# Optimization experiments

Hardware: AMD Instinct MI355X
Metric: run time of the kernel (lower is better)

## Reference

```python
import jax, jax.numpy as jnp
import numpy as np

N = 4096          # number of agents
TOP_K = 12        # config.TOP_K
OBS_RADIUS = 1.0  # config.OBS_RADIUS


def setup_inputs() -> dict:
    key = jax.random.key(0)
    ks = jax.random.split(key, 10)

    def lin(k, o, i):
        return jax.random.normal(k, (o, i), dtype=jnp.float32) * (1.0 / np.sqrt(i))

    x = jax.random.normal(ks[0], (N, N, 4), dtype=jnp.float32)
    r = jnp.asarray(0.25, dtype=jnp.float32)  # safety radius subtracted from d_norm
    W1 = lin(ks[1], 64, 6);   b1 = jax.random.normal(ks[2], (64,), jnp.float32) * 0.01
    W2 = lin(ks[3], 128, 64); b2 = jax.random.normal(ks[4], (128,), jnp.float32) * 0.01
    W3 = lin(ks[5], 64, 128); b3 = jax.random.normal(ks[6], (64,), jnp.float32) * 0.01
    W4 = lin(ks[7], 1, 64);   b4 = jax.random.normal(ks[8], (1,), jnp.float32) * 0.01
    return {"x": x, "r": r, "W1": W1, "b1": b1, "W2": W2, "b2": b2,
            "W3": W3, "b3": b3, "W4": W4, "b4": b4}


def reference(x, r, W1, b1, W2, b2, W3, b3, W4, b4):
    n = x.shape[0]
    # d_norm with eps added INSIDE the sum (matches torch: sum(x**2 + 1e-4))
    d_norm = jnp.sqrt(jnp.sum(x[:, :, :2] ** 2 + 0.0001, axis=2, keepdims=True))  # [n,n,1]
    eye = jnp.eye(n, dtype=x.dtype)[:, :, None]                                   # [n,n,1]
    xf = jnp.concatenate([x, eye, d_norm - r], axis=2)                            # [n,n,6]

    # remove_distant_agents: top-k nearest by 2D norm (eps 1e-6 inside sum)
    dn = jnp.sqrt(jnp.sum(xf[:, :, :2] ** 2 + 1e-06, axis=2))                     # [n,n]
    _, idx = jax.lax.top_k(-dn, TOP_K)                                            # [n,K]
    xg = jnp.take_along_axis(xf, idx[:, :, None], axis=1)                         # [n,K,6]

    dist = jnp.sqrt(jnp.sum(xg[:, :, :2] ** 2 + 0.0001, axis=2, keepdims=True))   # [n,K,1]
    mask = (dist <= OBS_RADIUS).astype(xg.dtype)

    # 1x1 Conv1d stack == per-neighbor MLP
    h = jax.nn.relu(jnp.einsum('nkc,oc->nko', xg, W1) + b1)
    h = jax.nn.relu(jnp.einsum('nkc,oc->nko', h, W2) + b2)
    h = jax.nn.relu(jnp.einsum('nkc,oc->nko', h, W3) + b3)
    out = (jnp.einsum('nkc,oc->nko', h, W4) + b4) * mask                          # [n,K,1]

    rows = jnp.broadcast_to(jnp.arange(n)[:, None], (n, TOP_K))
    indices = jnp.stack([rows, idx], axis=2).reshape(-1, 2)                       # [n*K,2]
    return out, mask, indices
```

## Files before the change

### kernel.cpp

```cpp
#include <hip/hip_runtime.h>

#define NN    4096
#define TOPK  12
#define NP    (NN * TOPK)
#define OFF_MASK (NP)
#define OFF_IDX  (2 * NP)

__device__ __forceinline__ unsigned long long bitonic64(unsigned long long key, int lane) {
    #pragma unroll
    for (int k = 2; k <= 64; k <<= 1) {
        #pragma unroll
        for (int jj = k >> 1; jj >= 1; jj >>= 1) {
            unsigned long long ok = __shfl_xor(key, jj, 64);
            bool keepMin = ((lane & k) == 0) == ((lane & jj) == 0);
            unsigned long long mn = (ok < key) ? ok : key;
            unsigned long long mx = (ok < key) ? key : ok;
            key = keepMin ? mn : mx;
        }
    }
    return key;
}

__global__ __launch_bounds__(256, 6) void topk_rows(const float* __restrict__ x,
                                                    float* __restrict__ out) {
    const int i    = blockIdx.x;
    const int t    = threadIdx.x;
    const int lane = t & 63;
    const int w    = t >> 6;
    const float4* x4 = (const float4*)x + (size_t)i * NN;

    float s[16];
    #pragma unroll
    for (int k = 0; k < 16; ++k) {
        float4 v = x4[(k << 8) + t];
        s[k] = v.x * v.x + v.y * v.y;
    }

    float bs = s[0]; int bj = t;
    #pragma unroll
    for (int k = 1; k < 16; ++k) {
        int j = (k << 8) + t;
        if (s[k] < bs) { bs = s[k]; bj = j; }
    }
    unsigned long long bk =
        ((unsigned long long)__float_as_uint(bs) << 32) | (unsigned)bj;

    __shared__ unsigned long long cand[64];
    __shared__ unsigned long long wtop[4 * TOPK];
    __shared__ float Tsh;
    __shared__ int   cnt[4];

    {
        unsigned long long key = bitonic64(bk, lane);
        if (lane < TOPK) wtop[w * TOPK + lane] = key;
    }
    __syncthreads();

    if (w == 0) {
        unsigned long long k2 = (lane < 4 * TOPK) ? wtop[lane] : ~0ULL;
        k2 = bitonic64(k2, lane);
        if (lane == TOPK - 1) Tsh = __uint_as_float((unsigned)(k2 >> 32));
    }
    __syncthreads();
    const float T = Tsh;

    int c = 0;
    #pragma unroll
    for (int k = 0; k < 16; ++k) c += (s[k] <= T) ? 1 : 0;

    int pfx = c;
    #pragma unroll
    for (int off = 1; off < 64; off <<= 1) {
        int o = __shfl_up(pfx, off, 64);
        if (lane >= off) pfx += o;
    }
    if (lane == 63) cnt[w] = pfx;
    __syncthreads();

    const int total = cnt[0] + cnt[1] + cnt[2] + cnt[3];

    if (total <= 64) {
        int base = 0;
        for (int ww = 0; ww < w; ++ww) base += cnt[ww];
        int o = base + (pfx - c);
        #pragma unroll
        for (int k = 0; k < 16; ++k) {
            if (s[k] <= T)
                cand[o++] = ((unsigned long long)__float_as_uint(s[k]) << 32)
                            | (unsigned)((k << 8) + t);
        }
        __syncthreads();

        if (w == 0) {
            unsigned long long k3 = (lane < total) ? cand[lane] : ~0ULL;
            k3 = bitonic64(k3, lane);
            if (lane < TOPK) {
                int   j  = (int)(k3 & 0xffffffffULL);
                float ss = __uint_as_float((unsigned)(k3 >> 32));
                float d  = sqrtf(ss + 2.0e-4f);
                float m  = (d <= 1.0f) ? 1.0f : 0.0f;
                int p = i * TOPK + lane;
                out[OFF_MASK + p]        = m;
                out[OFF_IDX + 2 * p]     = (float)i;
                out[OFF_IDX + 2 * p + 1] = (float)j;
            }
        }
        return;
    }

    unsigned long long mykey = ~0ULL;
    for (int it = 0; it < TOPK; ++it) {
        unsigned long long vk = bk;
        #pragma unroll
        for (int off = 1; off < 64; off <<= 1) {
            unsigned long long ok = __shfl_xor(vk, off, 64);
            vk = (ok < vk) ? ok : vk;
        }
        if (lane == it) mykey = vk;
        int wj = (int)(vk & 0xffffffffULL);
        if ((wj & 63) == lane) {
            int kk = wj >> 8;
            #pragma unroll
            for (int k = 0; k < 16; ++k)
                if (k == kk) s[k] = 3.0e38f;
            float nbs = s[0]; int nbj = t;
            #pragma unroll
            for (int k = 1; k < 16; ++k) {
                int j = (k << 8) + t;
                if (s[k] < nbs) { nbs = s[k]; nbj = j; }
            }
            bk = ((unsigned long long)__float_as_uint(nbs) << 32) | (unsigned)nbj;
        }
    }
    if (lane < TOPK) cand[w * TOPK + lane] = mykey;
    __syncthreads();

    if (w == 0) {
        unsigned long long k3 = (lane < 4 * TOPK) ? cand[lane] : ~0ULL;
        k3 = bitonic64(k3, lane);
        if (lane < TOPK) {
            int   j  = (int)(k3 & 0xffffffffULL);
            float ss = __uint_as_float((unsigned)(k3 >> 32));
            float d  = sqrtf(ss + 2.0e-4f);
            float m  = (d <= 1.0f) ? 1.0f : 0.0f;
            int p = i * TOPK + lane;
            out[OFF_MASK + p]        = m;
            out[OFF_IDX + 2 * p]     = (float)i;
            out[OFF_IDX + 2 * p + 1] = (float)j;
        }
    }
}

__global__ __launch_bounds__(512, 6) void mlp_block(
        const float* __restrict__ x, const float* __restrict__ rp,
        const float* __restrict__ W1, const float* __restrict__ b1,
        const float* __restrict__ W2, const float* __restrict__ b2,
        const float* __restrict__ W3, const float* __restrict__ b3,
        const float* __restrict__ W4, const float* __restrict__ b4,
        float* out) {
    __shared__ float h1s[64 * 64];
    __shared__ float h2s[128 * 64];
    __shared__ float p4s[8 * 64];

    const int t  = threadIdx.x;
    const int pl = t & 63;
    const int ch = __builtin_amdgcn_readfirstlane(t >> 6);
    const int p  = blockIdx.x * 64 + pl;
    const int i  = p / TOPK;
    const int j  = (int)out[OFF_IDX + 2 * p + 1];

    const float4 v = ((const float4*)x)[(size_t)i * NN + j];
    const float d  = sqrtf(v.x * v.x + v.y * v.y + 2.0e-4f);
    float xin[6];
    xin[0] = v.x; xin[1] = v.y; xin[2] = v.z; xin[3] = v.w;
    xin[4] = (i == j) ? 1.0f : 0.0f;
    xin[5] = d - rp[0];

    #pragma unroll
    for (int q = 0; q < 8; ++q) {
        int m = ch * 8 + q;
        const float* w = W1 + m * 6;
        float a = b1[m];
        #pragma unroll
        for (int c = 0; c < 6; ++c) a += w[c] * xin[c];
        h1s[m * 64 + pl] = fmaxf(a, 0.0f);
    }
    __syncthreads();

    float acc[16];
    #pragma unroll
    for (int q = 0; q < 16; ++q) acc[q] = b2[ch * 16 + q];
    for (int part = 0; part < 4; ++part) {
        float h1r[16];
        #pragma unroll
        for (int k = 0; k < 16; ++k) h1r[k] = h1s[(part * 16 + k) * 64 + pl];
        #pragma unroll
        for (int q = 0; q < 16; ++q) {
            const float* w = W2 + (ch * 16 + q) * 64 + part * 16;
            #pragma unroll
            for (int k = 0; k < 16; ++k) acc[q] += w[k] * h1r[k];
        }
    }
    #pragma unroll
    for (int q = 0; q < 16; ++q) h2s[(ch * 16 + q) * 64 + pl] = fmaxf(acc[q], 0.0f);
    __syncthreads();

    float h3[8];
    #pragma unroll
    for (int q = 0; q < 8; ++q) h3[q] = b3[ch * 8 + q];
    for (int part = 0; part < 8; ++part) {
        float h2r[16];
        #pragma unroll
        for (int k = 0; k < 16; ++k) h2r[k] = h2s[(part * 16 + k) * 64 + pl];
        #pragma unroll
        for (int q = 0; q < 8; ++q) {
            const float* w = W3 + (ch * 8 + q) * 128 + part * 16;
            #pragma unroll
            for (int k = 0; k < 16; ++k) h3[q] += w[k] * h2r[k];
        }
    }
    float partial = 0.0f;
    #pragma unroll
    for (int q = 0; q < 8; ++q) partial += W4[ch * 8 + q] * fmaxf(h3[q], 0.0f);
    p4s[ch * 64 + pl] = partial;
    __syncthreads();

    if (t < 64) {
        float s = b4[0];
        #pragma unroll
        for (int c = 0; c < 8; ++c) s += p4s[c * 64 + t];
        int pp = blockIdx.x * 64 + t;
        out[pp] = s * out[OFF_MASK + pp];
    }
}

extern "C" void kernel_launch(void* const* d_in, const int* in_sizes, int n_in,
                              void* d_out, int out_size, void* d_ws, size_t ws_size,
                              hipStream_t stream) {
    const float* x  = (const float*)d_in[0];
    const float* rp = (const float*)d_in[1];
    const float* W1 = (const float*)d_in[2];
    const float* b1 = (const float*)d_in[3];
    const float* W2 = (const float*)d_in[4];
    const float* b2 = (const float*)d_in[5];
    const float* W3 = (const float*)d_in[6];
    const float* b3 = (const float*)d_in[7];
    const float* W4 = (const float*)d_in[8];
    const float* b4 = (const float*)d_in[9];
    float* out = (float*)d_out;

    topk_rows<<<NN, 256, 0, stream>>>(x, out);
    mlp_block<<<NP / 64, 512, 0, stream>>>(x, rp, W1, b1, W2, b2, W3, b3, W4, b4, out);
}
```

Measured before the change: 405.2 us.

## Fuse top-k selection and per-neighbor MLP into a single kernel

Merges the top-k kernel and the MLP kernel into one launch, where each row's block runs the 12-neighbor MLP right after selection, using the top-12 keys kept in shared memory. This removes the second launch, the round trip of indices through global memory, and the gather re-read of x by a separate kernel. The cost is that only 192 of 256 threads work during the MLP, and the block keeps extra shared memory and registers, which may lower occupancy in the bandwidth-bound top-k phase.

```diff
diff --git a/kernel.cpp b/kernel.cpp
--- a/kernel.cpp
+++ b/kernel.cpp
@@ -21,8 +21,13 @@
     return key;
 }
 
-__global__ __launch_bounds__(256, 6) void topk_rows(const float* __restrict__ x,
-                                                    float* __restrict__ out) {
+__global__ __launch_bounds__(256, 6) void cbf_fused(
+        const float* __restrict__ x, const float* __restrict__ rp,
+        const float* __restrict__ W1, const float* __restrict__ b1,
+        const float* __restrict__ W2, const float* __restrict__ b2,
+        const float* __restrict__ W3, const float* __restrict__ b3,
+        const float* __restrict__ W4, const float* __restrict__ b4,
+        float* __restrict__ out) {
     const int i    = blockIdx.x;
     const int t    = threadIdx.x;
     const int lane = t & 63;
@@ -47,8 +52,12 @@
 
     __shared__ unsigned long long cand[64];
     __shared__ unsigned long long wtop[4 * TOPK];
+    __shared__ unsigned long long top12[TOPK];
     __shared__ float Tsh;
     __shared__ int   cnt[4];
+    __shared__ __align__(16) float h1sh[TOPK][68];
+    __shared__ __align__(16) float h2sh[TOPK][132];
+    __shared__ __align__(16) float p4sh[TOPK][16];
 
     {
         unsigned long long key = bitonic64(bk, lane);
@@ -95,6 +104,7 @@
             unsigned long long k3 = (lane < total) ? cand[lane] : ~0ULL;
             k3 = bitonic64(k3, lane);
             if (lane < TOPK) {
+                top12[lane] = k3;
                 int   j  = (int)(k3 & 0xffffffffULL);
                 float ss = __uint_as_float((unsigned)(k3 >> 32));
                 float d  = sqrtf(ss + 2.0e-4f);
@@ -105,132 +115,128 @@
                 out[OFF_IDX + 2 * p + 1] = (float)j;
             }
         }
-        return;
-    }
-
-    unsigned long long mykey = ~0ULL;
-    for (int it = 0; it < TOPK; ++it) {
-        unsigned long long vk = bk;
-        #pragma unroll
-        for (int off = 1; off < 64; off <<= 1) {
-            unsigned long long ok = __shfl_xor(vk, off, 64);
-            vk = (ok < vk) ? ok : vk;
-        }
-        if (lane == it) mykey = vk;
-        int wj = (int)(vk & 0xffffffffULL);
-        if ((wj & 63) == lane) {
-            int kk = wj >> 8;
-            #pragma unroll
-            for (int k = 0; k < 16; ++k)
-                if (k == kk) s[k] = 3.0e38f;
-            float nbs = s[0]; int nbj = t;
-            #pragma unroll
-            for (int k = 1; k < 16; ++k) {
-                int j = (k << 8) + t;
-                if (s[k] < nbs) { nbs = s[k]; nbj = j; }
-            }
-            bk = ((unsigned long long)__float_as_uint(nbs) << 32) | (unsigned)nbj;
-        }
-    }
-    if (lane < TOPK) cand[w * TOPK + lane] = mykey;
-    __syncthreads();
-
-    if (w == 0) {
-        unsigned long long k3 = (lane < 4 * TOPK) ? cand[lane] : ~0ULL;
-        k3 = bitonic64(k3, lane);
-        if (lane < TOPK) {
-            int   j  = (int)(k3 & 0xffffffffULL);
-            float ss = __uint_as_float((unsigned)(k3 >> 32));
-            float d  = sqrtf(ss + 2.0e-4f);
-            float m  = (d <= 1.0f) ? 1.0f : 0.0f;
-            int p = i * TOPK + lane;
-            out[OFF_MASK + p]        = m;
-            out[OFF_IDX + 2 * p]     = (float)i;
-            out[OFF_IDX + 2 * p + 1] = (float)j;
-        }
-    }
-}
-
-__global__ __launch_bounds__(512, 6) void mlp_block(
-        const float* __restrict__ x, const float* __restrict__ rp,
-        const float* __restrict__ W1, const float* __restrict__ b1,
-        const float* __restrict__ W2, const float* __restrict__ b2,
-        const float* __restrict__ W3, const float* __restrict__ b3,
-        const float* __restrict__ W4, const float* __restrict__ b4,
-        float* out) {
-    __shared__ float h1s[64 * 64];
-    __shared__ float h2s[128 * 64];
-    __shared__ float p4s[8 * 64];
-
-    const int t  = threadIdx.x;
-    const int pl = t & 63;
-    const int ch = __builtin_amdgcn_readfirstlane(t >> 6);
-    const int p  = blockIdx.x * 64 + pl;
-    const int i  = p / TOPK;
-    const int j  = (int)out[OFF_IDX + 2 * p + 1];
-
-    const float4 v = ((const float4*)x)[(size_t)i * NN + j];
-    const float d  = sqrtf(v.x * v.x + v.y * v.y + 2.0e-4f);
+    } else {
+        unsigned long long mykey = ~0ULL;
+        for (int it = 0; it < TOPK; ++it) {
+            unsigned long long vk = bk;
+            #pragma unroll
+            for (int off = 1; off < 64; off <<= 1) {
+                unsigned long long ok = __shfl_xor(vk, off, 64);
+                vk = (ok < vk) ? ok : vk;
+            }
+            if (lane == it) mykey = vk;
+            int wj = (int)(vk & 0xffffffffULL);
+            if ((wj & 63) == lane) {
+                int kk = wj >> 8;
+                #pragma unroll
+                for (int k = 0; k < 16; ++k)
+                    if (k == kk) s[k] = 3.0e38f;
+                float nbs = s[0]; int nbj = t;
+                #pragma unroll
+                for (int k = 1; k < 16; ++k) {
+                    int j = (k << 8) + t;
+                    if (s[k] < nbs) { nbs = s[k]; nbj = j; }
+                }
+                bk = ((unsigned long long)__float_as_uint(nbs) << 32) | (unsigned)nbj;
+            }
+        }
+        if (lane < TOPK) cand[w * TOPK + lane] = mykey;
+        __syncthreads();
+
+        if (w == 0) {
+            unsigned long long k3 = (lane < 4 * TOPK) ? cand[lane] : ~0ULL;
+            k3 = bitonic64(k3, lane);
+            if (lane < TOPK) {
+                top12[lane] = k3;
+                int   j  = (int)(k3 & 0xffffffffULL);
+                float ss = __uint_as_float((unsigned)(k3 >> 32));
+                float d  = sqrtf(ss + 2.0e-4f);
+                float m  = (d <= 1.0f) ? 1.0f : 0.0f;
+                int p = i * TOPK + lane;
+                out[OFF_MASK + p]        = m;
+                out[OFF_IDX + 2 * p]     = (float)i;
+                out[OFF_IDX + 2 * p + 1] = (float)j;
+            }
+        }
+    }
+    __syncthreads();
+
+    const bool act = (t < 192);
+    const int p = t >> 4;
+    const int l = t & 15;
+
     float xin[6];
-    xin[0] = v.x; xin[1] = v.y; xin[2] = v.z; xin[3] = v.w;
-    xin[4] = (i == j) ? 1.0f : 0.0f;
-    xin[5] = d - rp[0];
-
-    #pragma unroll
-    for (int q = 0; q < 8; ++q) {
-        int m = ch * 8 + q;
-        const float* w = W1 + m * 6;
-        float a = b1[m];
-        #pragma unroll
-        for (int c = 0; c < 6; ++c) a += w[c] * xin[c];
-        h1s[m * 64 + pl] = fmaxf(a, 0.0f);
-    }
-    __syncthreads();
-
-    float acc[16];
-    #pragma unroll
-    for (int q = 0; q < 16; ++q) acc[q] = b2[ch * 16 + q];
-    for (int part = 0; part < 4; ++part) {
-        float h1r[16];
-        #pragma unroll
-        for (int k = 0; k < 16; ++k) h1r[k] = h1s[(part * 16 + k) * 64 + pl];
-        #pragma unroll
-        for (int q = 0; q < 16; ++q) {
-            const float* w = W2 + (ch * 16 + q) * 64 + part * 16;
-            #pragma unroll
-            for (int k = 0; k < 16; ++k) acc[q] += w[k] * h1r[k];
-        }
-    }
-    #pragma unroll
-    for (int q = 0; q < 16; ++q) h2s[(ch * 16 + q) * 64 + pl] = fmaxf(acc[q], 0.0f);
-    __syncthreads();
-
-    float h3[8];
-    #pragma unroll
-    for (int q = 0; q < 8; ++q) h3[q] = b3[ch * 8 + q];
-    for (int part = 0; part < 8; ++part) {
-        float h2r[16];
-        #pragma unroll
-        for (int k = 0; k < 16; ++k) h2r[k] = h2s[(part * 16 + k) * 64 + pl];
-        #pragma unroll
-        for (int q = 0; q < 8; ++q) {
-            const float* w = W3 + (ch * 8 + q) * 128 + part * 16;
-            #pragma unroll
-            for (int k = 0; k < 16; ++k) h3[q] += w[k] * h2r[k];
-        }
-    }
-    float partial = 0.0f;
-    #pragma unroll
-    for (int q = 0; q < 8; ++q) partial += W4[ch * 8 + q] * fmaxf(h3[q], 0.0f);
-    p4s[ch * 64 + pl] = partial;
-    __syncthreads();
-
-    if (t < 64) {
-        float s = b4[0];
-        #pragma unroll
-        for (int c = 0; c < 8; ++c) s += p4s[c * 64 + t];
-        int pp = blockIdx.x * 64 + t;
-        out[pp] = s * out[OFF_MASK + pp];
+    float m = 0.0f;
+    if (act) {
+        const unsigned long long key = top12[p];
+        const int   j  = (int)(key & 0xffffffffULL);
+        const float ss = __uint_as_float((unsigned)(key >> 32));
+        const float d  = sqrtf(ss + 2.0e-4f);
+        m = (d <= 1.0f) ? 1.0f : 0.0f;
+
+        const float4 v = x4[j];
+        xin[0] = v.x; xin[1] = v.y; xin[2] = v.z; xin[3] = v.w;
+        xin[4] = (i == j) ? 1.0f : 0.0f;
+        xin[5] = d - rp[0];
+
+        #pragma unroll
+        for (int n = 0; n < 4; ++n) {
+            int q = l * 4 + n;
+            float a = b1[q];
+            #pragma unroll
+            for (int cc = 0; cc < 6; ++cc) a += W1[q * 6 + cc] * xin[cc];
+            h1sh[p][q] = fmaxf(a, 0.0f);
+        }
+    }
+    __syncthreads();
+
+    if (act) {
+        float acc2[8];
+        #pragma unroll
+        for (int n = 0; n < 8; ++n) acc2[n] = b2[l * 8 + n];
+        const float4* h1f4 = (const float4*)&h1sh[p][0];
+        const float4* w2f4 = (const float4*)W2;
+        #pragma unroll
+        for (int kk = 0; kk < 16; ++kk) {
+            float4 hv = h1f4[kk];
+            #pragma unroll
+            for (int n = 0; n < 8; ++n) {
+                float4 wv = w2f4[(l * 8 + n) * 16 + kk];
+                acc2[n] += wv.x * hv.x + wv.y * hv.y + wv.z * hv.z + wv.w * hv.w;
+            }
+        }
+        #pragma unroll
+        for (int n = 0; n < 8; ++n) h2sh[p][l * 8 + n] = fmaxf(acc2[n], 0.0f);
+    }
+    __syncthreads();
+
+    if (act) {
+        float acc3[4];
+        #pragma unroll
+        for (int n = 0; n < 4; ++n) acc3[n] = b3[l * 4 + n];
+        const float4* h2f4 = (const float4*)&h2sh[p][0];
+        const float4* w3f4 = (const float4*)W3;
+        #pragma unroll
+        for (int kk = 0; kk < 32; ++kk) {
+            float4 hv = h2f4[kk];
+            #pragma unroll
+            for (int n = 0; n < 4; ++n) {
+                float4 wv = w3f4[(l * 4 + n) * 32 + kk];
+                acc3[n] += wv.x * hv.x + wv.y * hv.y + wv.z * hv.z + wv.w * hv.w;
+            }
+        }
+        float partial = 0.0f;
+        #pragma unroll
+        for (int n = 0; n < 4; ++n) partial += W4[l * 4 + n] * fmaxf(acc3[n], 0.0f);
+        p4sh[p][l] = partial;
+    }
+    __syncthreads();
+
+    if (act && l == 0) {
+        float sum = b4[0];
+        #pragma unroll
+        for (int cc = 0; cc < 16; ++cc) sum += p4sh[p][cc];
+        out[i * TOPK + p] = sum * m;
     }
 }
 
@@ -249,6 +255,5 @@
     const float* b4 = (const float*)d_in[9];
     float* out = (float*)d_out;
 
-    topk_rows<<<NN, 256, 0, stream>>>(x, out);
-    mlp_block<<<NP / 64, 512, 0, stream>>>(x, rp, W1, b1, W2, b2, W3, b3, W4, b4, out);
+    cbf_fused<<<NN, 256, 0, stream>>>(x, rp, W1, b1, W2, b2, W3, b3, W4, b4, out);
 }
```

Result: slower. 713.4 us (+76.1%).

## Fuse top-k and MLP into one persistent pipelined kernel with flag handoff

Applied to the files above, without the earlier changes.

Merges the top-k row selection and the per-neighbor MLP into a single launch. Blocks are grouped so that 16 blocks compute top-k rows and 3 blocks run the MLP on those rows. The MLP blocks wait on per-element ready flags in workspace and recompute any row whose flag never arrives within a spin limit. This removes the second launch and the round trip of indices and mask through global memory, and lets the two stages overlap. In exchange it adds a memset, spin-wait polling, and halves MLP block width to 256 threads.

```diff
diff --git a/kernel.cpp b/kernel.cpp
--- a/kernel.cpp
+++ b/kernel.cpp
@@ -5,6 +5,10 @@
 #define NP    (NN * TOPK)
 #define OFF_MASK (NP)
 #define OFF_IDX  (2 * NP)
+
+#define GROUPS 256
+#define GRID   (GROUPS * 19)
+#define SPIN   10000
 
 __device__ __forceinline__ unsigned long long bitonic64(unsigned long long key, int lane) {
     #pragma unroll
@@ -21,10 +25,11 @@
     return key;
 }
 
-__global__ __launch_bounds__(256, 6) void topk_rows(const float* __restrict__ x,
-                                                    float* __restrict__ out) {
-    const int i    = blockIdx.x;
-    const int t    = threadIdx.x;
+__device__ __forceinline__ void topk_one_row(
+        const float* __restrict__ x, float* __restrict__ out,
+        int* __restrict__ wsf, int i, int t,
+        unsigned long long* cand, unsigned long long* wtop,
+        float* Tsh, int* cnt) {
     const int lane = t & 63;
     const int w    = t >> 6;
     const float4* x4 = (const float4*)x + (size_t)i * NN;
@@ -35,7 +40,6 @@
         float4 v = x4[(k << 8) + t];
         s[k] = v.x * v.x + v.y * v.y;
     }
-
     float bs = s[0]; int bj = t;
     #pragma unroll
     for (int k = 1; k < 16; ++k) {
@@ -45,11 +49,6 @@
     unsigned long long bk =
         ((unsigned long long)__float_as_uint(bs) << 32) | (unsigned)bj;
 
-    __shared__ unsigned long long cand[64];
-    __shared__ unsigned long long wtop[4 * TOPK];
-    __shared__ float Tsh;
-    __shared__ int   cnt[4];
-
     {
         unsigned long long key = bitonic64(bk, lane);
         if (lane < TOPK) wtop[w * TOPK + lane] = key;
@@ -59,15 +58,14 @@
     if (w == 0) {
         unsigned long long k2 = (lane < 4 * TOPK) ? wtop[lane] : ~0ULL;
         k2 = bitonic64(k2, lane);
-        if (lane == TOPK - 1) Tsh = __uint_as_float((unsigned)(k2 >> 32));
-    }
-    __syncthreads();
-    const float T = Tsh;
+        if (lane == TOPK - 1) *Tsh = __uint_as_float((unsigned)(k2 >> 32));
+    }
+    __syncthreads();
+    const float T = *Tsh;
 
     int c = 0;
     #pragma unroll
     for (int k = 0; k < 16; ++k) c += (s[k] <= T) ? 1 : 0;
-
     int pfx = c;
     #pragma unroll
     for (int off = 1; off < 64; off <<= 1) {
@@ -89,148 +87,193 @@
                 cand[o++] = ((unsigned long long)__float_as_uint(s[k]) << 32)
                             | (unsigned)((k << 8) + t);
         }
-        __syncthreads();
-
-        if (w == 0) {
-            unsigned long long k3 = (lane < total) ? cand[lane] : ~0ULL;
-            k3 = bitonic64(k3, lane);
-            if (lane < TOPK) {
-                int   j  = (int)(k3 & 0xffffffffULL);
-                float ss = __uint_as_float((unsigned)(k3 >> 32));
-                float d  = sqrtf(ss + 2.0e-4f);
-                float m  = (d <= 1.0f) ? 1.0f : 0.0f;
-                int p = i * TOPK + lane;
-                out[OFF_MASK + p]        = m;
-                out[OFF_IDX + 2 * p]     = (float)i;
-                out[OFF_IDX + 2 * p + 1] = (float)j;
-            }
-        }
-        return;
-    }
-
-    unsigned long long mykey = ~0ULL;
-    for (int it = 0; it < TOPK; ++it) {
-        unsigned long long vk = bk;
-        #pragma unroll
-        for (int off = 1; off < 64; off <<= 1) {
-            unsigned long long ok = __shfl_xor(vk, off, 64);
-            vk = (ok < vk) ? ok : vk;
-        }
-        if (lane == it) mykey = vk;
-        int wj = (int)(vk & 0xffffffffULL);
-        if ((wj & 63) == lane) {
-            int kk = wj >> 8;
-            #pragma unroll
-            for (int k = 0; k < 16; ++k)
-                if (k == kk) s[k] = 3.0e38f;
-            float nbs = s[0]; int nbj = t;
-            #pragma unroll
-            for (int k = 1; k < 16; ++k) {
-                int j = (k << 8) + t;
-                if (s[k] < nbs) { nbs = s[k]; nbj = j; }
-            }
-            bk = ((unsigned long long)__float_as_uint(nbs) << 32) | (unsigned)nbj;
-        }
-    }
-    if (lane < TOPK) cand[w * TOPK + lane] = mykey;
-    __syncthreads();
-
+    } else {
+        unsigned long long mykey = ~0ULL;
+        for (int it = 0; it < TOPK; ++it) {
+            unsigned long long vk = bk;
+            #pragma unroll
+            for (int off = 1; off < 64; off <<= 1) {
+                unsigned long long ok = __shfl_xor(vk, off, 64);
+                vk = (ok < vk) ? ok : vk;
+            }
+            if (lane == it) mykey = vk;
+            int wj = (int)(vk & 0xffffffffULL);
+            if ((wj & 63) == lane) {
+                int kk = wj >> 8;
+                #pragma unroll
+                for (int k = 0; k < 16; ++k)
+                    if (k == kk) s[k] = 3.0e38f;
+                float nbs = s[0]; int nbj = t;
+                #pragma unroll
+                for (int k = 1; k < 16; ++k) {
+                    int j = (k << 8) + t;
+                    if (s[k] < nbs) { nbs = s[k]; nbj = j; }
+                }
+                bk = ((unsigned long long)__float_as_uint(nbs) << 32) | (unsigned)nbj;
+            }
+        }
+        if (lane < TOPK) cand[w * TOPK + lane] = mykey;
+    }
+    __syncthreads();
+
+    const int n = (total <= 64) ? total : (4 * TOPK);
     if (w == 0) {
-        unsigned long long k3 = (lane < 4 * TOPK) ? cand[lane] : ~0ULL;
+        unsigned long long k3 = (lane < n) ? cand[lane] : ~0ULL;
         k3 = bitonic64(k3, lane);
         if (lane < TOPK) {
             int   j  = (int)(k3 & 0xffffffffULL);
             float ss = __uint_as_float((unsigned)(k3 >> 32));
             float d  = sqrtf(ss + 2.0e-4f);
-            float m  = (d <= 1.0f) ? 1.0f : 0.0f;
+            int   mb = (d <= 1.0f) ? 1 : 0;
             int p = i * TOPK + lane;
-            out[OFF_MASK + p]        = m;
+            out[OFF_MASK + p]        = (float)mb;
             out[OFF_IDX + 2 * p]     = (float)i;
             out[OFF_IDX + 2 * p + 1] = (float)j;
-        }
-    }
-}
-
-__global__ __launch_bounds__(512, 6) void mlp_block(
+            atomicExch(&wsf[i * TOPK + lane], (j << 2) | (mb << 1) | 1);
+        }
+    }
+}
+
+__global__ __launch_bounds__(256, 3) void cbf_pipe(
         const float* __restrict__ x, const float* __restrict__ rp,
         const float* __restrict__ W1, const float* __restrict__ b1,
         const float* __restrict__ W2, const float* __restrict__ b2,
         const float* __restrict__ W3, const float* __restrict__ b3,
         const float* __restrict__ W4, const float* __restrict__ b4,
-        float* out) {
-    __shared__ float h1s[64 * 64];
+        float* __restrict__ out, int* __restrict__ wsf) {
+    __shared__ __align__(16) float h1s[64 * 64];
     __shared__ float h2s[128 * 64];
     __shared__ float p4s[8 * 64];
-
-    const int t  = threadIdx.x;
+    __shared__ int   jmj[6 * TOPK];
+    __shared__ float jmm[6 * TOPK];
+    __shared__ int   nrdy[6];
+
+    unsigned long long* cand = (unsigned long long*)h1s;
+    unsigned long long* wtop = cand + 64;
+    float* Tsh = (float*)(wtop + 4 * TOPK);
+    int*   cnt = (int*)(Tsh + 1);
+
+    const int g    = blockIdx.x;
+    const int t    = threadIdx.x;
+    const int G    = g / 19;
+    const int role = g % 19;
+
+    if (role < 16) {
+        topk_one_row(x, out, wsf, G * 16 + role, t, cand, wtop, Tsh, cnt);
+        return;
+    }
+
+    const int mb = G * 3 + (role - 16);
+    const int r0 = (mb * 64) / TOPK;
+
+    if (t < 6) nrdy[t] = 0;
+    __syncthreads();
+    if (t < 72) {
+        int* f = &wsf[(r0 + t / TOPK) * TOPK + (t % TOPK)];
+        int v = 0;
+        for (int it = 0; it < SPIN; ++it) {
+            v = atomicAdd(f, 0);
+            if (v) break;
+            __builtin_amdgcn_s_sleep(4);
+        }
+        if (!v) nrdy[t / TOPK] = 1;
+    }
+    __syncthreads();
+    for (int r = 0; r < 6; ++r) {
+        if (nrdy[r]) {
+            topk_one_row(x, out, wsf, r0 + r, t, cand, wtop, Tsh, cnt);
+            __syncthreads();
+        }
+    }
+    if (t < 72) {
+        int v = atomicAdd(&wsf[(r0 + t / TOPK) * TOPK + (t % TOPK)], 0);
+        jmj[t] = v >> 2;
+        jmm[t] = ((v >> 1) & 1) ? 1.0f : 0.0f;
+    }
+    __syncthreads();
+
     const int pl = t & 63;
-    const int ch = __builtin_amdgcn_readfirstlane(t >> 6);
-    const int p  = blockIdx.x * 64 + pl;
-    const int i  = p / TOPK;
-    const int j  = (int)out[OFF_IDX + 2 * p + 1];
-
-    const float4 v = ((const float4*)x)[(size_t)i * NN + j];
+    const int wv = t >> 6;
+    const int p  = mb * 64 + pl;
+    const int ip = p / TOPK;
+    const int li = ip - r0;
+    const int kk = p % TOPK;
+    const int jj = jmj[li * TOPK + kk];
+
+    const float4 v = ((const float4*)x)[(size_t)ip * NN + jj];
     const float d  = sqrtf(v.x * v.x + v.y * v.y + 2.0e-4f);
     float xin[6];
     xin[0] = v.x; xin[1] = v.y; xin[2] = v.z; xin[3] = v.w;
-    xin[4] = (i == j) ? 1.0f : 0.0f;
+    xin[4] = (ip == jj) ? 1.0f : 0.0f;
     xin[5] = d - rp[0];
 
     #pragma unroll
-    for (int q = 0; q < 8; ++q) {
-        int m = ch * 8 + q;
-        const float* w = W1 + m * 6;
-        float a = b1[m];
-        #pragma unroll
-        for (int c = 0; c < 6; ++c) a += w[c] * xin[c];
-        h1s[m * 64 + pl] = fmaxf(a, 0.0f);
-    }
-    __syncthreads();
-
-    float acc[16];
-    #pragma unroll
-    for (int q = 0; q < 16; ++q) acc[q] = b2[ch * 16 + q];
-    for (int part = 0; part < 4; ++part) {
-        float h1r[16];
-        #pragma unroll
-        for (int k = 0; k < 16; ++k) h1r[k] = h1s[(part * 16 + k) * 64 + pl];
-        #pragma unroll
-        for (int q = 0; q < 16; ++q) {
-            const float* w = W2 + (ch * 16 + q) * 64 + part * 16;
-            #pragma unroll
-            for (int k = 0; k < 16; ++k) acc[q] += w[k] * h1r[k];
-        }
-    }
-    #pragma unroll
-    for (int q = 0; q < 16; ++q) h2s[(ch * 16 + q) * 64 + pl] = fmaxf(acc[q], 0.0f);
-    __syncthreads();
-
-    float h3[8];
-    #pragma unroll
-    for (int q = 0; q < 8; ++q) h3[q] = b3[ch * 8 + q];
-    for (int part = 0; part < 8; ++part) {
-        float h2r[16];
-        #pragma unroll
-        for (int k = 0; k < 16; ++k) h2r[k] = h2s[(part * 16 + k) * 64 + pl];
+    for (int half = 0; half < 2; ++half) {
+        const int ch = __builtin_amdgcn_readfirstlane(wv * 2 + half);
         #pragma unroll
         for (int q = 0; q < 8; ++q) {
-            const float* w = W3 + (ch * 8 + q) * 128 + part * 16;
-            #pragma unroll
-            for (int k = 0; k < 16; ++k) h3[q] += w[k] * h2r[k];
-        }
-    }
-    float partial = 0.0f;
-    #pragma unroll
-    for (int q = 0; q < 8; ++q) partial += W4[ch * 8 + q] * fmaxf(h3[q], 0.0f);
-    p4s[ch * 64 + pl] = partial;
+            int m = ch * 8 + q;
+            float a = b1[m];
+            #pragma unroll
+            for (int c2 = 0; c2 < 6; ++c2) a += W1[m * 6 + c2] * xin[c2];
+            h1s[m * 64 + pl] = fmaxf(a, 0.0f);
+        }
+    }
+    __syncthreads();
+
+    #pragma unroll
+    for (int half = 0; half < 2; ++half) {
+        const int ch = __builtin_amdgcn_readfirstlane(wv * 2 + half);
+        float acc[16];
+        #pragma unroll
+        for (int q = 0; q < 16; ++q) acc[q] = b2[ch * 16 + q];
+        for (int part = 0; part < 4; ++part) {
+            float h1r[16];
+            #pragma unroll
+            for (int k = 0; k < 16; ++k) h1r[k] = h1s[(part * 16 + k) * 64 + pl];
+            #pragma unroll
+            for (int q = 0; q < 16; ++q) {
+                const float* w2 = W2 + (ch * 16 + q) * 64 + part * 16;
+                #pragma unroll
+                for (int k = 0; k < 16; ++k) acc[q] += w2[k] * h1r[k];
+            }
+        }
+        #pragma unroll
+        for (int q = 0; q < 16; ++q) h2s[(ch * 16 + q) * 64 + pl] = fmaxf(acc[q], 0.0f);
+    }
+    __syncthreads();
+
+    #pragma unroll
+    for (int half = 0; half < 2; ++half) {
+        const int ch = __builtin_amdgcn_readfirstlane(wv * 2 + half);
+        float h3[8];
+        #pragma unroll
+        for (int q = 0; q < 8; ++q) h3[q] = b3[ch * 8 + q];
+        for (int part = 0; part < 8; ++part) {
+            float h2r[16];
+            #pragma unroll
+            for (int k = 0; k < 16; ++k) h2r[k] = h2s[(part * 16 + k) * 64 + pl];
+            #pragma unroll
+            for (int q = 0; q < 8; ++q) {
+                const float* w3 = W3 + (ch * 8 + q) * 128 + part * 16;
+                #pragma unroll
+                for (int k = 0; k < 16; ++k) h3[q] += w3[k] * h2r[k];
+            }
+        }
+        float partial = 0.0f;
+        #pragma unroll
+        for (int q = 0; q < 8; ++q) partial += W4[ch * 8 + q] * fmaxf(h3[q], 0.0f);
+        p4s[ch * 64 + pl] = partial;
+    }
     __syncthreads();
 
     if (t < 64) {
-        float s = b4[0];
-        #pragma unroll
-        for (int c = 0; c < 8; ++c) s += p4s[c * 64 + t];
-        int pp = blockIdx.x * 64 + t;
-        out[pp] = s * out[OFF_MASK + pp];
+        float s2 = b4[0];
+        #pragma unroll
+        for (int c2 = 0; c2 < 8; ++c2) s2 += p4s[c2 * 64 + t];
+        int pp  = mb * 64 + t;
+        int ip2 = pp / TOPK;
+        out[pp] = s2 * jmm[(ip2 - r0) * TOPK + (pp % TOPK)];
     }
 }
 
@@ -248,7 +291,9 @@
     const float* W4 = (const float*)d_in[8];
     const float* b4 = (const float*)d_in[9];
     float* out = (float*)d_out;
-
-    topk_rows<<<NN, 256, 0, stream>>>(x, out);
-    mlp_block<<<NP / 64, 512, 0, stream>>>(x, rp, W1, b1, W2, b2, W3, b3, W4, b4, out);
-}
+    int*   wsf = (int*)d_ws;
+
+    hipMemsetAsync(wsf, 0, NP * sizeof(int), stream);
+    cbf_pipe<<<GRID, 256, 0, stream>>>(x, rp, W1, b1, W2, b2, W3, b3, W4, b4,
+                                       out, wsf);
+}
```

Measured after the change: 421.7 us. +4.1%, slower.
